# Kernel tuning notes

Measured on AMD Instinct MI355X. Metric: run time of the kernel, lower is better.

Reference implementation:

```python
import jax, jax.numpy as jnp
import numpy as np

V = 16384  # points per mesh


def _nn_idx(q, r):
    """1-NN index into r for each row of q. q: [Vq,3], r: [Vr,3] -> [Vq] int32.

    Squared euclidean distance via ||q||^2 - 2 q.r + ||r||^2 (K=1 knn_points).
    """
    d = (jnp.sum(q * q, axis=-1, keepdims=True)
         - 2.0 * (q @ r.T)
         + jnp.sum(r * r, axis=-1)[None, :])  # [Vq, Vr]
    return jnp.argmin(d, axis=1)


def setup_inputs() -> dict:
    key = jax.random.key(0)
    k1, k2, k3, k4 = jax.random.split(key, 4)
    return {
        "pred_vertices": jax.random.normal(k1, (1, V, 3), dtype=jnp.float32),
        "trg_vertices": jax.random.normal(k2, (1, V, 3), dtype=jnp.float32),
        "pred_e": jax.random.normal(k3, (1, V, 3), dtype=jnp.float32),
        "trg_e": jax.random.normal(k4, (1, V, 3), dtype=jnp.float32),
    }


def reference(pred_vertices, trg_vertices, pred_e, trg_e):
    pv = pred_vertices[0]  # [V,3]
    tv = trg_vertices[0]   # [V,3]
    # knn_points runs under torch.no_grad() -> indices are constants
    trg2pred_idx = jax.lax.stop_gradient(_nn_idx(tv, pv))  # [V]
    pred2trg_idx = jax.lax.stop_gradient(_nn_idx(pv, tv))  # [V]
    loss_trg2pred = jnp.mean((trg_e - pred_e[:, trg2pred_idx, :]) ** 2)
    loss_pred2trg = jnp.mean((pred_e - trg_e[:, pred2trg_idx, :]) ** 2)
    return loss_trg2pred + loss_pred2trg
```

## Files before the change

### kernel.cpp

```cpp
#include <hip/hip_runtime.h>
#include <hip/hip_bf16.h>

#define NV 16384
#define NT 256
#define NTILES 512
#define RT_CHUNK 64
#define STG 16
#define RES_QPB 4
#define RES_BLOCKS (NV / RES_QPB)
#define NPART (2 * RES_BLOCKS)

typedef __attribute__((ext_vector_type(8))) short bf16x8;
typedef __attribute__((ext_vector_type(16))) float f32x16;

__device__ __forceinline__ short bf16bits(float f) {
    __hip_bfloat16 h = __float2bfloat16(f);
    return *reinterpret_cast<short*>(&h);
}
__device__ __forceinline__ float bf16tof(short s) {
    __hip_bfloat16 h = *reinterpret_cast<__hip_bfloat16*>(&s);
    return __bfloat162float(h);
}
__device__ __forceinline__ unsigned sortable(float f) {
    unsigned u = __float_as_uint(f);
    return (u & 0x80000000u) ? ~u : (u | 0x80000000u);
}
__device__ __forceinline__ float min3f(float a, float b, float c) {
    float r;
    asm("v_min3_f32 %0, %1, %2, %3" : "=v"(r) : "v"(a), "v"(b), "v"(c));
    return r;
}

__device__ __forceinline__ float tile_min32(const f32x16& a, const f32x16& b) {
    float t0 = min3f(a[0], a[1], a[2]);
    float t1 = min3f(a[3], a[4], a[5]);
    float t2 = min3f(a[6], a[7], a[8]);
    float t3 = min3f(a[9], a[10], a[11]);
    float t4 = min3f(a[12], a[13], a[14]);
    float t5 = min3f(a[15], b[0], b[1]);
    float t6 = min3f(b[2], b[3], b[4]);
    float t7 = min3f(b[5], b[6], b[7]);
    float t8 = min3f(b[8], b[9], b[10]);
    float t9 = min3f(b[11], b[12], b[13]);
    float ta = fminf(b[14], b[15]);
    float s0 = min3f(t0, t1, t2);
    float s1 = min3f(t3, t4, t5);
    float s2 = min3f(t6, t7, t8);
    float s3 = min3f(t9, ta, s0);
    return min3f(s1, s2, s3);
}

__global__ __launch_bounds__(NT) void prep_kernel(
    const float* __restrict__ pred_v, const float* __restrict__ trg_v,
    short* __restrict__ Apack, short* __restrict__ Bpack,
    unsigned long long* __restrict__ best)
{
    int gid = blockIdx.x * NT + threadIdx.x;
    if (gid < 2 * NV) best[gid] = 0xFFFFFFFFFFFFFFFFULL;

    int role = gid >> 16;
    int rem  = gid & 0xFFFF;
    int d    = rem >> 15;
    int t    = (rem >> 6) & 511;
    int l    = rem & 63;
    int pt   = l & 31;
    int half = l >> 5;

    const float* src = (role == 0) ? (d ? trg_v : pred_v)
                                   : (d ? pred_v : trg_v);
    int p = t * 32 + pt;
    float x = src[3 * p + 0], y = src[3 * p + 1], z = src[3 * p + 2];

    bf16x8 v;
    if (role == 0) {
        short hx = bf16bits(x), hy = bf16bits(y), hz = bf16bits(z);
        short lx = bf16bits(x - bf16tof(hx));
        short ly = bf16bits(y - bf16tof(hy));
        short lz = bf16bits(z - bf16tof(hz));
        float n  = 0.5f * fmaf(z, z, fmaf(y, y, x * x));
        short nh = bf16bits(n);
        short nl = bf16bits(n - bf16tof(nh));
        if (half == 0) { v[0]=hx; v[1]=hy; v[2]=hz; v[3]=lx; v[4]=ly; v[5]=lz; v[6]=hx; v[7]=hy; }
        else           { v[0]=hz; v[1]=nh; v[2]=nl; v[3]=0; v[4]=0; v[5]=0; v[6]=0; v[7]=0; }
    } else {
        short hx = bf16bits(x), hy = bf16bits(y), hz = bf16bits(z);
        short nhx = bf16bits(-x), nhy = bf16bits(-y), nhz = bf16bits(-z);
        short nlx = bf16bits(bf16tof(hx) - x);
        short nly = bf16bits(bf16tof(hy) - y);
        short nlz = bf16bits(bf16tof(hz) - z);
        const short one = 0x3F80;
        if (half == 0) { v[0]=nhx; v[1]=nhy; v[2]=nhz; v[3]=nhx; v[4]=nhy; v[5]=nhz; v[6]=nlx; v[7]=nly; }
        else           { v[0]=nlz; v[1]=one; v[2]=one; v[3]=0; v[4]=0; v[5]=0; v[6]=0; v[7]=0; }
    }
    short* dst = ((role == 0) ? Apack : Bpack) + (((size_t)(d * NTILES + t)) * 64 + l) * 8;
    *(bf16x8*)dst = v;
}

__global__ __launch_bounds__(NT) void nn_mfma_kernel(
    const short* __restrict__ Apack, const short* __restrict__ Bpack,
    unsigned long long* __restrict__ best)
{
    __shared__ short lds[STG * 512];
    const int tid = threadIdx.x, lane = tid & 63, w = tid >> 6;
    const int dir = blockIdx.z;
    const int qt0 = blockIdx.x * 8 + w * 2;
    const int rtb = blockIdx.y * RT_CHUNK;
    const size_t dbase = (size_t)dir * NTILES * 512;

    bf16x8 b0 = *(const bf16x8*)(Bpack + dbase + (size_t)qt0 * 512 + lane * 8);
    bf16x8 b1 = *(const bf16x8*)(Bpack + dbase + (size_t)(qt0 + 1) * 512 + lane * 8);

    float dmin0 = 1e30f, dmin1 = 1e30f;
    int bp0 = 0, bp1 = 0;

    for (int g = 0; g < RT_CHUNK / STG; g++) {
        __syncthreads();
        for (int t = w; t < STG; t += 4) {
            bf16x8 va = *(const bf16x8*)(Apack + dbase + (size_t)(rtb + g * STG + t) * 512 + lane * 8);
            *(bf16x8*)(&lds[t * 512 + lane * 8]) = va;
        }
        __syncthreads();
#pragma unroll
        for (int p = 0; p < STG / 2; p++) {
            bf16x8 a0 = *(const bf16x8*)(&lds[(2 * p) * 512 + lane * 8]);
            bf16x8 a1 = *(const bf16x8*)(&lds[(2 * p + 1) * 512 + lane * 8]);
            f32x16 zc = {};
            f32x16 c0 = __builtin_amdgcn_mfma_f32_32x32x16_bf16(a0, b0, zc, 0, 0, 0);
            f32x16 c1 = __builtin_amdgcn_mfma_f32_32x32x16_bf16(a1, b0, zc, 0, 0, 0);
            int pairid = blockIdx.y * 32 + g * (STG / 2) + p;
            float tm = tile_min32(c0, c1);
            bool lt = tm < dmin0; dmin0 = lt ? tm : dmin0; bp0 = lt ? pairid : bp0;
            f32x16 d0 = __builtin_amdgcn_mfma_f32_32x32x16_bf16(a0, b1, zc, 0, 0, 0);
            f32x16 d1 = __builtin_amdgcn_mfma_f32_32x32x16_bf16(a1, b1, zc, 0, 0, 0);
            tm = tile_min32(d0, d1);
            lt = tm < dmin1; dmin1 = lt ? tm : dmin1; bp1 = lt ? pairid : bp1;
        }
    }

    unsigned long long k0 = ((unsigned long long)sortable(dmin0) << 32) | (unsigned)bp0;
    unsigned long long k1 = ((unsigned long long)sortable(dmin1) << 32) | (unsigned)bp1;
    unsigned long long o0 = __shfl_xor(k0, 32); k0 = (o0 < k0) ? o0 : k0;
    unsigned long long o1 = __shfl_xor(k1, 32); k1 = (o1 < k1) ? o1 : k1;
    if (lane < 32) {
        atomicMin(&best[dir * NV + qt0 * 32 + lane], k0);
        atomicMin(&best[dir * NV + (qt0 + 1) * 32 + lane], k1);
    }
}

__global__ __launch_bounds__(NT) void resolve_loss_kernel(
    const float* __restrict__ pred_v, const float* __restrict__ trg_v,
    const float* __restrict__ pred_e, const float* __restrict__ trg_e,
    const unsigned long long* __restrict__ best, float* __restrict__ partials)
{
    const int dir = blockIdx.y;
    const float* qpts = dir ? pred_v : trg_v;
    const float* rpts = dir ? trg_v : pred_v;
    const float* qe_b = dir ? pred_e : trg_e;
    const float* re_b = dir ? trg_e : pred_e;
    const unsigned long long* b = best + dir * NV;

    const int tid = threadIdx.x, lane = tid & 63, wv = tid >> 6;
    const int q = blockIdx.x * RES_QPB + wv;

    const int pair = (int)(unsigned)(b[q] & 0xFFFFFFFFULL);
    const int i = pair * 64 + lane;

    float nqx = -qpts[3 * q + 0], nqy = -qpts[3 * q + 1], nqz = -qpts[3 * q + 2];
    float x = rpts[3 * i + 0], y = rpts[3 * i + 1], z = rpts[3 * i + 2];
    float rw = 0.5f * fmaf(z, z, fmaf(y, y, x * x));
    float s = fmaf(nqx, x, rw);
    s = fmaf(nqy, y, s);
    s = fmaf(nqz, z, s);

    unsigned long long key = ((unsigned long long)sortable(s) << 32) | (unsigned)i;
#pragma unroll
    for (int off = 32; off > 0; off >>= 1) {
        unsigned long long o = __shfl_xor(key, off);
        key = (o < key) ? o : key;
    }

    __shared__ float wsum[RES_QPB];
    if (lane == 0) {
        int j = (int)(unsigned)(key & 0xFFFFFFFFULL);
        float dx = qe_b[3 * q + 0] - re_b[3 * j + 0];
        float dy = qe_b[3 * q + 1] - re_b[3 * j + 1];
        float dz = qe_b[3 * q + 2] - re_b[3 * j + 2];
        wsum[wv] = fmaf(dx, dx, fmaf(dy, dy, dz * dz));
    }
    __syncthreads();
    if (tid == 0)
        partials[dir * RES_BLOCKS + blockIdx.x] =
            (wsum[0] + wsum[1]) + (wsum[2] + wsum[3]);
}

__global__ __launch_bounds__(NT) void final_kernel(
    const float* __restrict__ partials, float* __restrict__ out)
{
    const int tid = threadIdx.x;
    float acc = 0.0f;
#pragma unroll
    for (int t = 0; t < NPART / NT; t++) acc += partials[t * NT + tid];
    __shared__ float red[NT];
    red[tid] = acc;
    __syncthreads();
    for (int s = NT / 2; s > 0; s >>= 1) {
        if (tid < s) red[tid] += red[tid + s];
        __syncthreads();
    }
    if (tid == 0) out[0] = red[0] * (1.0f / 49152.0f);
}

extern "C" void kernel_launch(void* const* d_in, const int* in_sizes, int n_in,
                              void* d_out, int out_size, void* d_ws, size_t ws_size,
                              hipStream_t stream) {
    const float* pred_v = (const float*)d_in[0];
    const float* trg_v  = (const float*)d_in[1];
    const float* pred_e = (const float*)d_in[2];
    const float* trg_e  = (const float*)d_in[3];
    float* out = (float*)d_out;

    unsigned long long* best = (unsigned long long*)d_ws;
    short* Apack = (short*)(best + 2 * NV);
    short* Bpack = Apack + 2 * NTILES * 512;
    float* partials = (float*)(Bpack + 2 * NTILES * 512);

    prep_kernel<<<(2 * 2 * NTILES * 64) / NT, NT, 0, stream>>>(pred_v, trg_v, Apack, Bpack, best);

    nn_mfma_kernel<<<dim3(NTILES / 8, NTILES / RT_CHUNK, 2), NT, 0, stream>>>(Apack, Bpack, best);

    resolve_loss_kernel<<<dim3(RES_BLOCKS, 2), NT, 0, stream>>>(
        pred_v, trg_v, pred_e, trg_e, best, partials);

    final_kernel<<<1, NT, 0, stream>>>(partials, out);
}
```

Measured before the change: 47.16 us.

## Fuse bf16 packing into NN kernel and replace atomics with per-chunk results

```diff
diff --git a/kernel.cpp b/kernel.cpp
--- a/kernel.cpp
+++ b/kernel.cpp
@@ -5,7 +5,8 @@
 #define NT 256
 #define NTILES 512
 #define RT_CHUNK 64
-#define STG 16
+#define NCHUNK (NTILES / RT_CHUNK)
+#define STG 32
 #define RES_QPB 4
 #define RES_BLOCKS (NV / RES_QPB)
 #define NPART (2 * RES_BLOCKS)
@@ -30,110 +31,92 @@
     asm("v_min3_f32 %0, %1, %2, %3" : "=v"(r) : "v"(a), "v"(b), "v"(c));
     return r;
 }
-
-__device__ __forceinline__ float tile_min32(const f32x16& a, const f32x16& b) {
-    float t0 = min3f(a[0], a[1], a[2]);
-    float t1 = min3f(a[3], a[4], a[5]);
-    float t2 = min3f(a[6], a[7], a[8]);
-    float t3 = min3f(a[9], a[10], a[11]);
-    float t4 = min3f(a[12], a[13], a[14]);
-    float t5 = min3f(a[15], b[0], b[1]);
-    float t6 = min3f(b[2], b[3], b[4]);
-    float t7 = min3f(b[5], b[6], b[7]);
-    float t8 = min3f(b[8], b[9], b[10]);
-    float t9 = min3f(b[11], b[12], b[13]);
-    float ta = fminf(b[14], b[15]);
-    float s0 = min3f(t0, t1, t2);
-    float s1 = min3f(t3, t4, t5);
-    float s2 = min3f(t6, t7, t8);
-    float s3 = min3f(t9, ta, s0);
-    return min3f(s1, s2, s3);
-}
-
-__global__ __launch_bounds__(NT) void prep_kernel(
+__device__ __forceinline__ float tree16(const f32x16& c) {
+    float t0 = min3f(c[0], c[1], c[2]);
+    float t1 = min3f(c[3], c[4], c[5]);
+    float t2 = min3f(c[6], c[7], c[8]);
+    float t3 = min3f(c[9], c[10], c[11]);
+    float t4 = min3f(c[12], c[13], c[14]);
+    float s0 = min3f(t0, t1, c[15]);
+    float s1 = min3f(t2, t3, t4);
+    return fminf(s0, s1);
+}
+
+__device__ __forceinline__ bf16x8 make_a(float x, float y, float z, int half) {
+    short hx = bf16bits(x), hy = bf16bits(y), hz = bf16bits(z);
+    short lx = bf16bits(x - bf16tof(hx));
+    short ly = bf16bits(y - bf16tof(hy));
+    short lz = bf16bits(z - bf16tof(hz));
+    float n  = 0.5f * fmaf(z, z, fmaf(y, y, x * x));
+    short nh = bf16bits(n);
+    short nl = bf16bits(n - bf16tof(nh));
+    bf16x8 v;
+    v[0] = half ? hz : hx;  v[1] = half ? nh : hy;
+    v[2] = half ? nl : hz;  v[3] = half ? (short)0 : lx;
+    v[4] = half ? (short)0 : ly;  v[5] = half ? (short)0 : lz;
+    v[6] = half ? (short)0 : hx;  v[7] = half ? (short)0 : hy;
+    return v;
+}
+__device__ __forceinline__ bf16x8 make_b(float x, float y, float z, int half) {
+    short hx = bf16bits(x), hy = bf16bits(y), hz = bf16bits(z);
+    short nhx = bf16bits(-x), nhy = bf16bits(-y), nhz = bf16bits(-z);
+    short nlx = bf16bits(bf16tof(hx) - x);
+    short nly = bf16bits(bf16tof(hy) - y);
+    short nlz = bf16bits(bf16tof(hz) - z);
+    const short one = 0x3F80;
+    bf16x8 v;
+    v[0] = half ? nlz : nhx;  v[1] = half ? one : nhy;
+    v[2] = half ? one : nhz;  v[3] = half ? (short)0 : nhx;
+    v[4] = half ? (short)0 : nhy;  v[5] = half ? (short)0 : nhz;
+    v[6] = half ? (short)0 : nlx;  v[7] = half ? (short)0 : nly;
+    return v;
+}
+
+__global__ __launch_bounds__(NT, 4) void nn_mfma_kernel(
     const float* __restrict__ pred_v, const float* __restrict__ trg_v,
-    short* __restrict__ Apack, short* __restrict__ Bpack,
-    unsigned long long* __restrict__ best)
-{
-    int gid = blockIdx.x * NT + threadIdx.x;
-    if (gid < 2 * NV) best[gid] = 0xFFFFFFFFFFFFFFFFULL;
-
-    int role = gid >> 16;
-    int rem  = gid & 0xFFFF;
-    int d    = rem >> 15;
-    int t    = (rem >> 6) & 511;
-    int l    = rem & 63;
-    int pt   = l & 31;
-    int half = l >> 5;
-
-    const float* src = (role == 0) ? (d ? trg_v : pred_v)
-                                   : (d ? pred_v : trg_v);
-    int p = t * 32 + pt;
-    float x = src[3 * p + 0], y = src[3 * p + 1], z = src[3 * p + 2];
-
-    bf16x8 v;
-    if (role == 0) {
-        short hx = bf16bits(x), hy = bf16bits(y), hz = bf16bits(z);
-        short lx = bf16bits(x - bf16tof(hx));
-        short ly = bf16bits(y - bf16tof(hy));
-        short lz = bf16bits(z - bf16tof(hz));
-        float n  = 0.5f * fmaf(z, z, fmaf(y, y, x * x));
-        short nh = bf16bits(n);
-        short nl = bf16bits(n - bf16tof(nh));
-        if (half == 0) { v[0]=hx; v[1]=hy; v[2]=hz; v[3]=lx; v[4]=ly; v[5]=lz; v[6]=hx; v[7]=hy; }
-        else           { v[0]=hz; v[1]=nh; v[2]=nl; v[3]=0; v[4]=0; v[5]=0; v[6]=0; v[7]=0; }
-    } else {
-        short hx = bf16bits(x), hy = bf16bits(y), hz = bf16bits(z);
-        short nhx = bf16bits(-x), nhy = bf16bits(-y), nhz = bf16bits(-z);
-        short nlx = bf16bits(bf16tof(hx) - x);
-        short nly = bf16bits(bf16tof(hy) - y);
-        short nlz = bf16bits(bf16tof(hz) - z);
-        const short one = 0x3F80;
-        if (half == 0) { v[0]=nhx; v[1]=nhy; v[2]=nhz; v[3]=nhx; v[4]=nhy; v[5]=nhz; v[6]=nlx; v[7]=nly; }
-        else           { v[0]=nlz; v[1]=one; v[2]=one; v[3]=0; v[4]=0; v[5]=0; v[6]=0; v[7]=0; }
-    }
-    short* dst = ((role == 0) ? Apack : Bpack) + (((size_t)(d * NTILES + t)) * 64 + l) * 8;
-    *(bf16x8*)dst = v;
-}
-
-__global__ __launch_bounds__(NT) void nn_mfma_kernel(
-    const short* __restrict__ Apack, const short* __restrict__ Bpack,
-    unsigned long long* __restrict__ best)
+    unsigned long long* __restrict__ results)
 {
     __shared__ short lds[STG * 512];
     const int tid = threadIdx.x, lane = tid & 63, w = tid >> 6;
     const int dir = blockIdx.z;
+    const float* qpts = dir ? pred_v : trg_v;
+    const float* rpts = dir ? trg_v : pred_v;
     const int qt0 = blockIdx.x * 8 + w * 2;
     const int rtb = blockIdx.y * RT_CHUNK;
-    const size_t dbase = (size_t)dir * NTILES * 512;
-
-    bf16x8 b0 = *(const bf16x8*)(Bpack + dbase + (size_t)qt0 * 512 + lane * 8);
-    bf16x8 b1 = *(const bf16x8*)(Bpack + dbase + (size_t)(qt0 + 1) * 512 + lane * 8);
+    const int half = lane >> 5;
+
+    const int qp0 = qt0 * 32 + (lane & 31);
+    bf16x8 b0 = make_b(qpts[3 * qp0 + 0], qpts[3 * qp0 + 1], qpts[3 * qp0 + 2], half);
+    bf16x8 b1 = make_b(qpts[3 * (qp0 + 32) + 0], qpts[3 * (qp0 + 32) + 1],
+                       qpts[3 * (qp0 + 32) + 2], half);
 
     float dmin0 = 1e30f, dmin1 = 1e30f;
     int bp0 = 0, bp1 = 0;
+    const f32x16 zc = {};
 
     for (int g = 0; g < RT_CHUNK / STG; g++) {
         __syncthreads();
-        for (int t = w; t < STG; t += 4) {
-            bf16x8 va = *(const bf16x8*)(Apack + dbase + (size_t)(rtb + g * STG + t) * 512 + lane * 8);
-            *(bf16x8*)(&lds[t * 512 + lane * 8]) = va;
+        for (int s = tid; s < STG * 64; s += NT) {
+            int t = s >> 6, l = s & 63;
+            int rp = (rtb + g * STG + t) * 32 + (l & 31);
+            bf16x8 va = make_a(rpts[3 * rp + 0], rpts[3 * rp + 1], rpts[3 * rp + 2], l >> 5);
+            *(bf16x8*)(&lds[t * 512 + l * 8]) = va;
         }
         __syncthreads();
-#pragma unroll
+#pragma unroll 2
         for (int p = 0; p < STG / 2; p++) {
             bf16x8 a0 = *(const bf16x8*)(&lds[(2 * p) * 512 + lane * 8]);
+            f32x16 c0 = __builtin_amdgcn_mfma_f32_32x32x16_bf16(a0, b0, zc, 0, 0, 0);
+            f32x16 c1 = __builtin_amdgcn_mfma_f32_32x32x16_bf16(a0, b1, zc, 0, 0, 0);
+            float u0 = tree16(c0), u1 = tree16(c1);
             bf16x8 a1 = *(const bf16x8*)(&lds[(2 * p + 1) * 512 + lane * 8]);
-            f32x16 zc = {};
-            f32x16 c0 = __builtin_amdgcn_mfma_f32_32x32x16_bf16(a0, b0, zc, 0, 0, 0);
-            f32x16 c1 = __builtin_amdgcn_mfma_f32_32x32x16_bf16(a1, b0, zc, 0, 0, 0);
-            int pairid = blockIdx.y * 32 + g * (STG / 2) + p;
-            float tm = tile_min32(c0, c1);
-            bool lt = tm < dmin0; dmin0 = lt ? tm : dmin0; bp0 = lt ? pairid : bp0;
-            f32x16 d0 = __builtin_amdgcn_mfma_f32_32x32x16_bf16(a0, b1, zc, 0, 0, 0);
+            f32x16 d0 = __builtin_amdgcn_mfma_f32_32x32x16_bf16(a1, b0, zc, 0, 0, 0);
             f32x16 d1 = __builtin_amdgcn_mfma_f32_32x32x16_bf16(a1, b1, zc, 0, 0, 0);
-            tm = tile_min32(d0, d1);
-            lt = tm < dmin1; dmin1 = lt ? tm : dmin1; bp1 = lt ? pairid : bp1;
+            float m0 = fminf(u0, tree16(d0));
+            float m1 = fminf(u1, tree16(d1));
+            int pid = blockIdx.y * (RT_CHUNK / 2) + g * (STG / 2) + p;
+            bool lt0 = m0 < dmin0; dmin0 = lt0 ? m0 : dmin0; bp0 = lt0 ? pid : bp0;
+            bool lt1 = m1 < dmin1; dmin1 = lt1 ? m1 : dmin1; bp1 = lt1 ? pid : bp1;
         }
     }
 
@@ -142,27 +125,35 @@
     unsigned long long o0 = __shfl_xor(k0, 32); k0 = (o0 < k0) ? o0 : k0;
     unsigned long long o1 = __shfl_xor(k1, 32); k1 = (o1 < k1) ? o1 : k1;
     if (lane < 32) {
-        atomicMin(&best[dir * NV + qt0 * 32 + lane], k0);
-        atomicMin(&best[dir * NV + (qt0 + 1) * 32 + lane], k1);
+        size_t base = ((size_t)dir * NCHUNK + blockIdx.y) * NV;
+        results[base + qt0 * 32 + lane] = k0;
+        results[base + (qt0 + 1) * 32 + lane] = k1;
     }
 }
 
 __global__ __launch_bounds__(NT) void resolve_loss_kernel(
     const float* __restrict__ pred_v, const float* __restrict__ trg_v,
     const float* __restrict__ pred_e, const float* __restrict__ trg_e,
-    const unsigned long long* __restrict__ best, float* __restrict__ partials)
+    const unsigned long long* __restrict__ results, float* __restrict__ partials)
 {
     const int dir = blockIdx.y;
     const float* qpts = dir ? pred_v : trg_v;
     const float* rpts = dir ? trg_v : pred_v;
     const float* qe_b = dir ? pred_e : trg_e;
     const float* re_b = dir ? trg_e : pred_e;
-    const unsigned long long* b = best + dir * NV;
 
     const int tid = threadIdx.x, lane = tid & 63, wv = tid >> 6;
     const int q = blockIdx.x * RES_QPB + wv;
 
-    const int pair = (int)(unsigned)(b[q] & 0xFFFFFFFFULL);
+    unsigned long long key = 0xFFFFFFFFFFFFFFFFULL;
+    if (lane < NCHUNK)
+        key = results[((size_t)dir * NCHUNK + lane) * NV + q];
+    unsigned long long o;
+    o = __shfl_xor(key, 4); key = (o < key) ? o : key;
+    o = __shfl_xor(key, 2); key = (o < key) ? o : key;
+    o = __shfl_xor(key, 1); key = (o < key) ? o : key;
+    key = __shfl(key, 0);
+    const int pair = (int)(unsigned)(key & 0xFFFFFFFFULL);
     const int i = pair * 64 + lane;
 
     float nqx = -qpts[3 * q + 0], nqy = -qpts[3 * q + 1], nqz = -qpts[3 * q + 2];
@@ -172,16 +163,16 @@
     s = fmaf(nqy, y, s);
     s = fmaf(nqz, z, s);
 
-    unsigned long long key = ((unsigned long long)sortable(s) << 32) | (unsigned)i;
+    unsigned long long kk = ((unsigned long long)sortable(s) << 32) | (unsigned)i;
 #pragma unroll
     for (int off = 32; off > 0; off >>= 1) {
-        unsigned long long o = __shfl_xor(key, off);
-        key = (o < key) ? o : key;
+        unsigned long long t = __shfl_xor(kk, off);
+        kk = (t < kk) ? t : kk;
     }
 
     __shared__ float wsum[RES_QPB];
     if (lane == 0) {
-        int j = (int)(unsigned)(key & 0xFFFFFFFFULL);
+        int j = (int)(unsigned)(kk & 0xFFFFFFFFULL);
         float dx = qe_b[3 * q + 0] - re_b[3 * j + 0];
         float dy = qe_b[3 * q + 1] - re_b[3 * j + 1];
         float dz = qe_b[3 * q + 2] - re_b[3 * j + 2];
@@ -219,17 +210,13 @@
     const float* trg_e  = (const float*)d_in[3];
     float* out = (float*)d_out;
 
-    unsigned long long* best = (unsigned long long*)d_ws;
-    short* Apack = (short*)(best + 2 * NV);
-    short* Bpack = Apack + 2 * NTILES * 512;
-    float* partials = (float*)(Bpack + 2 * NTILES * 512);
-
-    prep_kernel<<<(2 * 2 * NTILES * 64) / NT, NT, 0, stream>>>(pred_v, trg_v, Apack, Bpack, best);
-
-    nn_mfma_kernel<<<dim3(NTILES / 8, NTILES / RT_CHUNK, 2), NT, 0, stream>>>(Apack, Bpack, best);
+    unsigned long long* results = (unsigned long long*)d_ws;
+    float* partials = (float*)(results + 2 * NCHUNK * NV);
+
+    nn_mfma_kernel<<<dim3(NTILES / 8, NCHUNK, 2), NT, 0, stream>>>(pred_v, trg_v, results);
 
     resolve_loss_kernel<<<dim3(RES_BLOCKS, 2), NT, 0, stream>>>(
-        pred_v, trg_v, pred_e, trg_e, best, partials);
+        pred_v, trg_v, pred_e, trg_e, results, partials);
 
     final_kernel<<<1, NT, 0, stream>>>(partials, out);
 }
```

Measured after the change: 39.06 us. 17.2% less time.
